# Optimization experiments

Measured on AMD Instinct MI355X. Metric: run time of the kernel, lower is better.

The kernel has to match this reference:

```python
import jax, jax.numpy as jnp
import numpy as np

N = 100000   # nodes
E = 1600000  # edges
IN = 32
HID = 64
OUT = 1

def setup_inputs() -> dict:
    key = jax.random.key(0)
    ks = jax.random.split(key, 16)
    x = jax.random.normal(ks[0], (N, IN), jnp.float32)
    edge_index = jax.random.randint(ks[1], (2, E), 0, N, dtype=jnp.int32)
    def lin(k, fi, fo):
        return jax.random.normal(k, (fi, fo), jnp.float32) / np.sqrt(fi)
    # SAGEConv params per layer: Wn/bn for aggregated neighbors (lin_l), Wr for root (lin_r, no bias)
    Wn0 = lin(ks[2], IN, HID);  bn0 = jnp.zeros((HID,), jnp.float32); Wr0 = lin(ks[3], IN, HID)
    Wn1 = lin(ks[4], HID, HID); bn1 = jnp.zeros((HID,), jnp.float32); Wr1 = lin(ks[5], HID, HID)
    Wn2 = lin(ks[6], HID, HID); bn2 = jnp.zeros((HID,), jnp.float32); Wr2 = lin(ks[7], HID, HID)
    # predictor MLP
    Wp1 = lin(ks[8], HID, HID); bp1 = jnp.zeros((HID,), jnp.float32)
    Wp2 = lin(ks[9], HID, OUT); bp2 = jnp.zeros((OUT,), jnp.float32)
    return dict(x=x, edge_index=edge_index,
                Wn0=Wn0, bn0=bn0, Wr0=Wr0,
                Wn1=Wn1, bn1=bn1, Wr1=Wr1,
                Wn2=Wn2, bn2=bn2, Wr2=Wr2,
                Wp1=Wp1, bp1=bp1, Wp2=Wp2, bp2=bp2)

def reference(x, edge_index, Wn0, bn0, Wr0, Wn1, bn1, Wr1, Wn2, bn2, Wr2, Wp1, bp1, Wp2, bp2):
    src, dst = edge_index[0], edge_index[1]
    n = x.shape[0]
    # mean-aggregation normalization (nodes with no in-edges get 0, as in PyG)
    cnt = jax.ops.segment_sum(jnp.ones(src.shape, x.dtype), dst, num_segments=n)
    inv = jnp.where(cnt > 0, 1.0 / jnp.maximum(cnt, 1.0), 0.0)[:, None]

    def sage(h, Wn, bn, Wr):
        agg = jax.ops.segment_sum(h[src], dst, num_segments=n) * inv  # [N, d]
        return agg @ Wn + bn + h @ Wr

    h = jax.nn.relu(sage(x, Wn0, bn0, Wr0))
    h = jax.nn.relu(sage(h, Wn1, bn1, Wr1))
    h = sage(h, Wn2, bn2, Wr2)  # no activation after last GNN layer
    h = jax.nn.relu(h @ Wp1 + bp1)
    return jax.nn.sigmoid(h @ Wp2 + bp2)
```

## Files before the change

kernel.cpp:

```cpp
#include <hip/hip_runtime.h>
#include <math.h>

#define NN 100000
#define EE 1600000
#define HID 64
#define BKT 391
#define SLAB 5504
#define CHUNK 4096
#define NWG ((EE + CHUNK - 1) / CHUNK)
#define TB (NN / 16)

typedef _Float16 f16;
typedef _Float16 f16x2 __attribute__((ext_vector_type(2)));

__device__ __forceinline__ f16x2 u2h(unsigned u) { return __builtin_bit_cast(f16x2, u); }
__device__ __forceinline__ unsigned h2u(f16x2 h) { return __builtin_bit_cast(unsigned, h); }

#if defined(__has_builtin) && __has_builtin(__builtin_amdgcn_fdot2)
__device__ __forceinline__ float dot2(f16x2 a, f16x2 b, float c) {
    return __builtin_amdgcn_fdot2(a, b, c, false);
}
#else
__device__ __forceinline__ float dot2(f16x2 a, f16x2 b, float c) {
    c = fmaf((float)a.x, (float)b.x, c);
    return fmaf((float)a.y, (float)b.y, c);
}
#endif


__global__ void mt_kernel(const int* __restrict__ src, const int* __restrict__ dst,
                          int* __restrict__ bfill, unsigned* __restrict__ pairs,
                          const float* __restrict__ h,
                          const float* __restrict__ Wn, const float* __restrict__ bn,
                          const float* __restrict__ Wr,
                          f16* __restrict__ hn, f16* __restrict__ hrb,
                          const float* __restrict__ Wn1, const float* __restrict__ Wr1,
                          const float* __restrict__ Wn2, const float* __restrict__ Wr2,
                          const float* __restrict__ Wp1, unsigned* __restrict__ w16) {
    __shared__ int lc[BKT];
    __shared__ int lbase[BKT];
    int t = threadIdx.x;

    if (blockIdx.x < NWG) {
        for (int b = t; b < BKT; b += 256) lc[b] = 0;
        __syncthreads();
        int base = blockIdx.x * CHUNK;
        int myd[CHUNK / 256];
#pragma unroll
        for (int j = 0; j < CHUNK / 256; ++j) {
            int i = base + j * 256 + t;
            myd[j] = (i < EE) ? dst[i] : -1;
            if (myd[j] >= 0) atomicAdd(&lc[myd[j] >> 8], 1);
        }
        __syncthreads();
        for (int b = t; b < BKT; b += 256) {
            int c = lc[b];
            if (c) {
                int ofs = atomicAdd(&bfill[b], c);
                if (ofs + c > SLAB) ofs = SLAB - c;
                lbase[b] = b * SLAB + ofs;
            }
        }
        __syncthreads();
        for (int b = t; b < BKT; b += 256) lc[b] = 0;
        __syncthreads();
#pragma unroll
        for (int j = 0; j < CHUNK / 256; ++j) {
            int i = base + j * 256 + t;
            if (myd[j] >= 0) {
                int b = myd[j] >> 8;
                int r = atomicAdd(&lc[b], 1);
                pairs[lbase[b] + r] = (unsigned)src[i] | ((unsigned)(myd[j] & 255) << 24);
            }
        }
        return;
    }

    int bb = blockIdx.x - NWG;

    if (bb < 40) {
        int id = bb * 256 + t;
        int mat = id >> 11;
        int p = (id >> 6) & 31;
        int j = id & 63;
        const float* W = (mat == 0) ? Wn1 : (mat == 1) ? Wr1 :
                         (mat == 2) ? Wn2 : (mat == 3) ? Wr2 : Wp1;
        f16x2 v;
        v.x = (f16)W[(2 * p) * HID + j];
        v.y = (f16)W[(2 * p + 1) * HID + j];
        w16[id] = h2u(v);
    }

    int lane = t & 63;
    int wid = (bb * 256 + t) >> 6;
    int m0 = __builtin_amdgcn_readfirstlane(wid << 2);
    const float* h0 = h + (size_t)m0 * 32;

    float an0 = 0.f, an1 = 0.f, an2 = 0.f, an3 = 0.f;
    float ar0 = 0.f, ar1 = 0.f, ar2 = 0.f, ar3 = 0.f;
#pragma unroll
    for (int k = 0; k < 32; ++k) {
        float wn = Wn[k * HID + lane];
        float wr = Wr[k * HID + lane];
        float hk0 = h0[k], hk1 = h0[32 + k], hk2 = h0[64 + k], hk3 = h0[96 + k];
        an0 = fmaf(hk0, wn, an0); ar0 = fmaf(hk0, wr, ar0);
        an1 = fmaf(hk1, wn, an1); ar1 = fmaf(hk1, wr, ar1);
        an2 = fmaf(hk2, wn, an2); ar2 = fmaf(hk2, wr, ar2);
        an3 = fmaf(hk3, wn, an3); ar3 = fmaf(hk3, wr, ar3);
    }
    float b = bn[lane];
    size_t o = (size_t)m0 * HID + lane;
    hn[o] = (f16)an0; hn[o + HID] = (f16)an1;
    hn[o + 2 * HID] = (f16)an2; hn[o + 3 * HID] = (f16)an3;
    hrb[o] = (f16)(ar0 + b); hrb[o + HID] = (f16)(ar1 + b);
    hrb[o + 2 * HID] = (f16)(ar2 + b); hrb[o + 3 * HID] = (f16)(ar3 + b);
}


__global__ void build_kernel(const unsigned* __restrict__ pairs,
                             const int* __restrict__ bfill,
                             int* __restrict__ rs, int* __restrict__ re,
                             float* __restrict__ inv, int* __restrict__ col) {
    __shared__ unsigned s_pk[SLAB];
    __shared__ int ncnt[256];
    __shared__ int nexcl[256];
    int b = blockIdx.x;
    int t = threadIdx.x;
    int s0 = b * SLAB;
    int ce = bfill[b]; if (ce > SLAB) ce = SLAB;
    ncnt[t] = 0;
    for (int e = t; e < ce; e += 256) s_pk[e] = pairs[s0 + e];
    __syncthreads();
    for (int e = t; e < ce; e += 256) atomicAdd(&ncnt[s_pk[e] >> 24], 1);
    __syncthreads();
    int c = ncnt[t];
    nexcl[t] = c;
    __syncthreads();
    for (int off = 1; off < 256; off <<= 1) {
        int u = (t >= off) ? nexcl[t - off] : 0;
        __syncthreads();
        nexcl[t] += u;
        __syncthreads();
    }
    int excl = nexcl[t] - c;
    int node = (b << 8) + t;
    if (node < NN) {
        rs[node] = s0 + excl;
        re[node] = s0 + excl + c;
        inv[node] = (c > 0) ? (1.0f / (float)c) : 0.0f;
    }
    __syncthreads();
    nexcl[t] = excl;
    ncnt[t] = 0;
    __syncthreads();
    for (int e = t; e < ce; e += 256) {
        unsigned pk = s_pk[e];
        int d = pk >> 24;
        int r = atomicAdd(&ncnt[d], 1);
        col[s0 + nexcl[d] + r] = (int)(pk & 0xFFFFFFu);
    }
}


__device__ __forceinline__ void qgather(const uint2* __restrict__ rp,
                                        const int* __restrict__ col,
                                        int e, int en, int fl,
                                        f16x2& s0, f16x2& s1) {
    while (e + 8 <= en) {
        int c0 = col[e],     c1 = col[e + 1], c2 = col[e + 2], c3 = col[e + 3];
        int c4 = col[e + 4], c5 = col[e + 5], c6 = col[e + 6], c7 = col[e + 7];
        uint2 v0 = rp[(size_t)c0 * 16 + fl];
        uint2 v1 = rp[(size_t)c1 * 16 + fl];
        uint2 v2 = rp[(size_t)c2 * 16 + fl];
        uint2 v3 = rp[(size_t)c3 * 16 + fl];
        uint2 v4 = rp[(size_t)c4 * 16 + fl];
        uint2 v5 = rp[(size_t)c5 * 16 + fl];
        uint2 v6 = rp[(size_t)c6 * 16 + fl];
        uint2 v7 = rp[(size_t)c7 * 16 + fl];
        s0 += u2h(v0.x); s1 += u2h(v0.y);
        s0 += u2h(v1.x); s1 += u2h(v1.y);
        s0 += u2h(v2.x); s1 += u2h(v2.y);
        s0 += u2h(v3.x); s1 += u2h(v3.y);
        s0 += u2h(v4.x); s1 += u2h(v4.y);
        s0 += u2h(v5.x); s1 += u2h(v5.y);
        s0 += u2h(v6.x); s1 += u2h(v6.y);
        s0 += u2h(v7.x); s1 += u2h(v7.y);
        e += 8;
    }
    if (e + 4 <= en) {
        int c0 = col[e], c1 = col[e + 1], c2 = col[e + 2], c3 = col[e + 3];
        uint2 v0 = rp[(size_t)c0 * 16 + fl];
        uint2 v1 = rp[(size_t)c1 * 16 + fl];
        uint2 v2 = rp[(size_t)c2 * 16 + fl];
        uint2 v3 = rp[(size_t)c3 * 16 + fl];
        s0 += u2h(v0.x); s1 += u2h(v0.y);
        s0 += u2h(v1.x); s1 += u2h(v1.y);
        s0 += u2h(v2.x); s1 += u2h(v2.y);
        s0 += u2h(v3.x); s1 += u2h(v3.y);
        e += 4;
    }
    while (e < en) {
        uint2 v = rp[(size_t)col[e] * 16 + fl];
        s0 += u2h(v.x); s1 += u2h(v.y);
        ++e;
    }
}


__global__ void gt_kernel(const f16* __restrict__ An,
                          const int* __restrict__ rs, const int* __restrict__ re,
                          const int* __restrict__ col, const float* __restrict__ inv,
                          f16* C,
                          const unsigned* __restrict__ Wn16, const float* __restrict__ bn,
                          const unsigned* __restrict__ Wr16,
                          f16* __restrict__ Aout) {
    int lane = threadIdx.x & 63;
    int wid = (blockIdx.x * blockDim.x + threadIdx.x) >> 6;
    int m0 = wid << 2;
    int m = m0 + (lane >> 4);
    int fl = lane & 15;

    f16x2 s0 = (f16x2)0, s1 = (f16x2)0;
    qgather((const uint2*)An, col, rs[m], re[m], fl, s0, s1);

    float iv = inv[m];
    uint2 cur = ((const uint2*)C)[(size_t)m * 16 + fl];
    f16x2 q0 = u2h(cur.x), q1 = u2h(cur.y);
    f16x2 hA, hB;
    hA.x = (f16)fmaxf(fmaf((float)s0.x, iv, (float)q0.x), 0.f);
    hA.y = (f16)fmaxf(fmaf((float)s0.y, iv, (float)q0.y), 0.f);
    hB.x = (f16)fmaxf(fmaf((float)s1.x, iv, (float)q1.x), 0.f);
    hB.y = (f16)fmaxf(fmaf((float)s1.y, iv, (float)q1.y), 0.f);
    unsigned hx = h2u(hA), hy = h2u(hB);

    float an[4] = {0.f, 0.f, 0.f, 0.f};
    float ar[4] = {0.f, 0.f, 0.f, 0.f};
#pragma unroll
    for (int kk = 0; kk < 16; ++kk) {
        f16x2 wnA = u2h(Wn16[(2 * kk) * HID + lane]);
        f16x2 wnB = u2h(Wn16[(2 * kk + 1) * HID + lane]);
        f16x2 wrA = u2h(Wr16[(2 * kk) * HID + lane]);
        f16x2 wrB = u2h(Wr16[(2 * kk + 1) * HID + lane]);
#pragma unroll
        for (int n = 0; n < 4; ++n) {
            f16x2 px = u2h(__shfl(hx, (n << 4) + kk));
            f16x2 py = u2h(__shfl(hy, (n << 4) + kk));
            an[n] = dot2(px, wnA, an[n]);
            an[n] = dot2(py, wnB, an[n]);
            ar[n] = dot2(px, wrA, ar[n]);
            ar[n] = dot2(py, wrB, ar[n]);
        }
    }
    float b = bn[lane];
    size_t o = (size_t)m0 * HID + lane;
#pragma unroll
    for (int n = 0; n < 4; ++n) {
        Aout[o + n * HID] = (f16)an[n];
        C[o + n * HID] = (f16)(ar[n] + b);
    }
}


__global__ void gh_kernel(const f16* __restrict__ An,
                          const int* __restrict__ rs, const int* __restrict__ re,
                          const int* __restrict__ col, const float* __restrict__ inv,
                          const f16* __restrict__ C,
                          const unsigned* __restrict__ Wp116, const float* __restrict__ bp1,
                          const float* __restrict__ Wp2, const float* __restrict__ bp2,
                          float* __restrict__ out) {
    int lane = threadIdx.x & 63;
    int wid = (blockIdx.x * blockDim.x + threadIdx.x) >> 6;
    int m0 = wid << 2;
    int m = m0 + (lane >> 4);
    int fl = lane & 15;

    f16x2 s0 = (f16x2)0, s1 = (f16x2)0;
    qgather((const uint2*)An, col, rs[m], re[m], fl, s0, s1);

    float iv = inv[m];
    uint2 cur = ((const uint2*)C)[(size_t)m * 16 + fl];
    f16x2 q0 = u2h(cur.x), q1 = u2h(cur.y);
    f16x2 hA, hB;
    hA.x = (f16)fmaf((float)s0.x, iv, (float)q0.x);
    hA.y = (f16)fmaf((float)s0.y, iv, (float)q0.y);
    hB.x = (f16)fmaf((float)s1.x, iv, (float)q1.x);
    hB.y = (f16)fmaf((float)s1.y, iv, (float)q1.y);
    unsigned hx = h2u(hA), hy = h2u(hB);

    float tn[4] = {0.f, 0.f, 0.f, 0.f};
#pragma unroll
    for (int kk = 0; kk < 16; ++kk) {
        f16x2 wA = u2h(Wp116[(2 * kk) * HID + lane]);
        f16x2 wB = u2h(Wp116[(2 * kk + 1) * HID + lane]);
#pragma unroll
        for (int n = 0; n < 4; ++n) {
            f16x2 px = u2h(__shfl(hx, (n << 4) + kk));
            f16x2 py = u2h(__shfl(hy, (n << 4) + kk));
            tn[n] = dot2(px, wA, tn[n]);
            tn[n] = dot2(py, wB, tn[n]);
        }
    }
    float b = bp1[lane], w2v = Wp2[lane];
    float r0 = fmaxf(tn[0] + b, 0.f) * w2v;
    float r1 = fmaxf(tn[1] + b, 0.f) * w2v;
    float r2 = fmaxf(tn[2] + b, 0.f) * w2v;
    float r3 = fmaxf(tn[3] + b, 0.f) * w2v;
#pragma unroll
    for (int off = 32; off > 0; off >>= 1) {
        r0 += __shfl_xor(r0, off);
        r1 += __shfl_xor(r1, off);
        r2 += __shfl_xor(r2, off);
        r3 += __shfl_xor(r3, off);
    }
    if (lane == 0) {
        float bb = bp2[0];
        out[m0]     = 1.f / (1.f + expf(-(r0 + bb)));
        out[m0 + 1] = 1.f / (1.f + expf(-(r1 + bb)));
        out[m0 + 2] = 1.f / (1.f + expf(-(r2 + bb)));
        out[m0 + 3] = 1.f / (1.f + expf(-(r3 + bb)));
    }
}

extern "C" void kernel_launch(void* const* d_in, const int* in_sizes, int n_in,
                              void* d_out, int out_size, void* d_ws, size_t ws_size,
                              hipStream_t stream) {
    const float* x   = (const float*)d_in[0];
    const int* eidx  = (const int*)d_in[1];
    const float* Wn0 = (const float*)d_in[2];
    const float* bn0 = (const float*)d_in[3];
    const float* Wr0 = (const float*)d_in[4];
    const float* Wn1 = (const float*)d_in[5];
    const float* bn1 = (const float*)d_in[6];
    const float* Wr1 = (const float*)d_in[7];
    const float* Wn2 = (const float*)d_in[8];
    const float* bn2 = (const float*)d_in[9];
    const float* Wr2 = (const float*)d_in[10];
    const float* Wp1 = (const float*)d_in[11];
    const float* bp1 = (const float*)d_in[12];
    const float* Wp2 = (const float*)d_in[13];
    const float* bp2 = (const float*)d_in[14];
    float* out = (float*)d_out;

    const int* src = eidx;
    const int* dst = eidx + EE;

    char* w = (char*)d_ws;
    size_t off = 0;
    auto carve = [&](size_t bytes) -> void* {
        void* p = w + off;
        off = (off + bytes + 255) & ~(size_t)255;
        return p;
    };
    int*   rsA    = (int*)carve((size_t)NN * 4);
    int*   reA    = (int*)carve((size_t)NN * 4);
    float* inv    = (float*)carve((size_t)NN * 4);
    int*   col    = (int*)carve((size_t)BKT * SLAB * 4);
    int*   bfill  = (int*)carve((size_t)BKT * 4);
    unsigned* w16 = (unsigned*)carve((size_t)5 * 2048 * 4);
    f16*   A0     = (f16*)carve((size_t)NN * HID * 2);
    f16*   A1     = (f16*)carve((size_t)NN * HID * 2);
    f16*   C      = (f16*)carve((size_t)NN * HID * 2);
    unsigned* pairs = (unsigned*)carve((size_t)BKT * SLAB * 4);
    (void)ws_size;

    unsigned* Wn1_16 = w16;
    unsigned* Wr1_16 = w16 + 2048;
    unsigned* Wn2_16 = w16 + 4096;
    unsigned* Wr2_16 = w16 + 6144;
    unsigned* Wp1_16 = w16 + 8192;

    hipMemsetAsync(bfill, 0, (size_t)BKT * 4, stream);

    mt_kernel<<<NWG + TB, 256, 0, stream>>>(src, dst, bfill, pairs,
                                            x, Wn0, bn0, Wr0, A0, C,
                                            Wn1, Wr1, Wn2, Wr2, Wp1, w16);
    build_kernel<<<BKT, 256, 0, stream>>>(pairs, bfill, rsA, reA, inv, col);

    gt_kernel<<<TB, 256, 0, stream>>>(A0, rsA, reA, col, inv, C, Wn1_16, bn1, Wr1_16, A1);
    gt_kernel<<<TB, 256, 0, stream>>>(A1, rsA, reA, col, inv, C, Wn2_16, bn2, Wr2_16, A0);
    gh_kernel<<<TB, 256, 0, stream>>>(A0, rsA, reA, col, inv, C, Wp1_16, bp1, Wp2, bp2, out);
}
```

Baseline: 278.7 us.

## Replace bucketed pair staging with per-node count, scan, and atomic scatter CSR build

The CSR build no longer stages packed (src, local dst) pairs into per-bucket slabs and sorts them in shared memory. It now does three passes: a global atomic histogram of destination degrees, a per-bucket block scan that writes row starts and cursors, and a scatter pass that places each source with a global atomicAdd on its destination cursor. This drops the pairs buffer and the shared-memory sort, at the cost of 1.6M global atomics spread over 100k counters in each of two passes, plus one extra kernel launch. Neighbor order inside a row becomes nondeterministic, which changes the fp16 accumulation order.

Result: slower. 439.9 us (+57.9%).

```diff
diff --git a/kernel.cpp b/kernel.cpp
--- a/kernel.cpp
+++ b/kernel.cpp
@@ -6,8 +6,8 @@
 #define HID 64
 #define BKT 391
 #define SLAB 5504
-#define CHUNK 4096
-#define NWG ((EE + CHUNK - 1) / CHUNK)
+#define CHUNK_S 1024
+#define NCB ((EE + CHUNK_S - 1) / CHUNK_S)
 #define TB (NN / 16)
 
 typedef _Float16 f16;
@@ -28,8 +28,7 @@
 #endif
 
 
-__global__ void mt_kernel(const int* __restrict__ src, const int* __restrict__ dst,
-                          int* __restrict__ bfill, unsigned* __restrict__ pairs,
+__global__ void ct_kernel(const int* __restrict__ dst, int* __restrict__ cnt,
                           const float* __restrict__ h,
                           const float* __restrict__ Wn, const float* __restrict__ bn,
                           const float* __restrict__ Wr,
@@ -37,46 +36,19 @@
                           const float* __restrict__ Wn1, const float* __restrict__ Wr1,
                           const float* __restrict__ Wn2, const float* __restrict__ Wr2,
                           const float* __restrict__ Wp1, unsigned* __restrict__ w16) {
-    __shared__ int lc[BKT];
-    __shared__ int lbase[BKT];
     int t = threadIdx.x;
 
-    if (blockIdx.x < NWG) {
-        for (int b = t; b < BKT; b += 256) lc[b] = 0;
-        __syncthreads();
-        int base = blockIdx.x * CHUNK;
-        int myd[CHUNK / 256];
-#pragma unroll
-        for (int j = 0; j < CHUNK / 256; ++j) {
+    if (blockIdx.x < NCB) {
+        int base = blockIdx.x * CHUNK_S;
+#pragma unroll
+        for (int j = 0; j < CHUNK_S / 256; ++j) {
             int i = base + j * 256 + t;
-            myd[j] = (i < EE) ? dst[i] : -1;
-            if (myd[j] >= 0) atomicAdd(&lc[myd[j] >> 8], 1);
-        }
-        __syncthreads();
-        for (int b = t; b < BKT; b += 256) {
-            int c = lc[b];
-            if (c) {
-                int ofs = atomicAdd(&bfill[b], c);
-                if (ofs + c > SLAB) ofs = SLAB - c;
-                lbase[b] = b * SLAB + ofs;
-            }
-        }
-        __syncthreads();
-        for (int b = t; b < BKT; b += 256) lc[b] = 0;
-        __syncthreads();
-#pragma unroll
-        for (int j = 0; j < CHUNK / 256; ++j) {
-            int i = base + j * 256 + t;
-            if (myd[j] >= 0) {
-                int b = myd[j] >> 8;
-                int r = atomicAdd(&lc[b], 1);
-                pairs[lbase[b] + r] = (unsigned)src[i] | ((unsigned)(myd[j] & 255) << 24);
-            }
+            if (i < EE) atomicAdd(&cnt[dst[i]], 1);
         }
         return;
     }
 
-    int bb = blockIdx.x - NWG;
+    int bb = blockIdx.x - NCB;
 
     if (bb < 40) {
         int id = bb * 256 + t;
@@ -117,47 +89,49 @@
 }
 
 
-__global__ void build_kernel(const unsigned* __restrict__ pairs,
-                             const int* __restrict__ bfill,
-                             int* __restrict__ rs, int* __restrict__ re,
-                             float* __restrict__ inv, int* __restrict__ col) {
-    __shared__ unsigned s_pk[SLAB];
-    __shared__ int ncnt[256];
-    __shared__ int nexcl[256];
+__global__ void scan_kernel(const int* __restrict__ cnt,
+                            int* __restrict__ rs, int* __restrict__ re,
+                            float* __restrict__ inv, int* __restrict__ cursor) {
+    __shared__ int sc[256];
     int b = blockIdx.x;
     int t = threadIdx.x;
-    int s0 = b * SLAB;
-    int ce = bfill[b]; if (ce > SLAB) ce = SLAB;
-    ncnt[t] = 0;
-    for (int e = t; e < ce; e += 256) s_pk[e] = pairs[s0 + e];
-    __syncthreads();
-    for (int e = t; e < ce; e += 256) atomicAdd(&ncnt[s_pk[e] >> 24], 1);
-    __syncthreads();
-    int c = ncnt[t];
-    nexcl[t] = c;
+    int node = (b << 8) + t;
+    int c = (node < NN) ? cnt[node] : 0;
+    sc[t] = c;
     __syncthreads();
     for (int off = 1; off < 256; off <<= 1) {
-        int u = (t >= off) ? nexcl[t - off] : 0;
+        int u = (t >= off) ? sc[t - off] : 0;
         __syncthreads();
-        nexcl[t] += u;
+        sc[t] += u;
         __syncthreads();
     }
-    int excl = nexcl[t] - c;
-    int node = (b << 8) + t;
+    int excl = sc[t] - c;
     if (node < NN) {
-        rs[node] = s0 + excl;
-        re[node] = s0 + excl + c;
+        int s0 = b * SLAB;
+        int cap = s0 + SLAB;
+        int start = s0 + excl; if (start > cap) start = cap;
+        int end = start + c;   if (end > cap) end = cap;
+        rs[node] = start;
+        re[node] = end;
         inv[node] = (c > 0) ? (1.0f / (float)c) : 0.0f;
-    }
-    __syncthreads();
-    nexcl[t] = excl;
-    ncnt[t] = 0;
-    __syncthreads();
-    for (int e = t; e < ce; e += 256) {
-        unsigned pk = s_pk[e];
-        int d = pk >> 24;
-        int r = atomicAdd(&ncnt[d], 1);
-        col[s0 + nexcl[d] + r] = (int)(pk & 0xFFFFFFu);
+        cursor[node] = start;
+    }
+}
+
+
+__global__ void scat_kernel(const int* __restrict__ src, const int* __restrict__ dst,
+                            int* __restrict__ cursor, int* __restrict__ col) {
+    int t = threadIdx.x;
+    int base = blockIdx.x * CHUNK_S;
+#pragma unroll
+    for (int j = 0; j < CHUNK_S / 256; ++j) {
+        int i = base + j * 256 + t;
+        if (i < EE) {
+            int d = dst[i];
+            int slot = atomicAdd(&cursor[d], 1);
+            int cap = ((d >> 8) + 1) * SLAB;
+            if (slot < cap) col[slot] = src[i];
+        }
     }
 }
 
@@ -355,12 +329,12 @@
     int*   reA    = (int*)carve((size_t)NN * 4);
     float* inv    = (float*)carve((size_t)NN * 4);
     int*   col    = (int*)carve((size_t)BKT * SLAB * 4);
-    int*   bfill  = (int*)carve((size_t)BKT * 4);
+    int*   cnt    = (int*)carve((size_t)NN * 4);
+    int*   cursor = (int*)carve((size_t)NN * 4);
     unsigned* w16 = (unsigned*)carve((size_t)5 * 2048 * 4);
     f16*   A0     = (f16*)carve((size_t)NN * HID * 2);
     f16*   A1     = (f16*)carve((size_t)NN * HID * 2);
     f16*   C      = (f16*)carve((size_t)NN * HID * 2);
-    unsigned* pairs = (unsigned*)carve((size_t)BKT * SLAB * 4);
     (void)ws_size;
 
     unsigned* Wn1_16 = w16;
@@ -369,12 +343,13 @@
     unsigned* Wr2_16 = w16 + 6144;
     unsigned* Wp1_16 = w16 + 8192;
 
-    hipMemsetAsync(bfill, 0, (size_t)BKT * 4, stream);
-
-    mt_kernel<<<NWG + TB, 256, 0, stream>>>(src, dst, bfill, pairs,
+    hipMemsetAsync(cnt, 0, (size_t)NN * 4, stream);
+
+    ct_kernel<<<NCB + TB, 256, 0, stream>>>(dst, cnt,
                                             x, Wn0, bn0, Wr0, A0, C,
                                             Wn1, Wr1, Wn2, Wr2, Wp1, w16);
-    build_kernel<<<BKT, 256, 0, stream>>>(pairs, bfill, rsA, reA, inv, col);
+    scan_kernel<<<BKT, 256, 0, stream>>>(cnt, rsA, reA, inv, cursor);
+    scat_kernel<<<NCB, 256, 0, stream>>>(src, dst, cursor, col);
 
     gt_kernel<<<TB, 256, 0, stream>>>(A0, rsA, reA, col, inv, C, Wn1_16, bn1, Wr1_16, A1);
     gt_kernel<<<TB, 256, 0, stream>>>(A1, rsA, reA, col, inv, C, Wn2_16, bn2, Wr2_16, A0);
```
